# Optimization experiments

Hardware: AMD Instinct MI355X
Metric: run time of the kernel (lower is better)

Reference implementation:

```python
import jax, jax.numpy as jnp
import numpy as np

FD, NH, SP, GS = 256, 4, 2, 80.0
E = FD // NH
SP3 = SP ** 3


def _bilinear(plane, uv):
    # plane: [B,C,H,W], uv: [B,N,2] in [0,1] -> [B,C,N] (align_corners=True style)
    B, C, H, W = plane.shape
    x = jnp.clip(uv[..., 0], 0.0, 1.0) * (W - 1)
    y = jnp.clip(uv[..., 1], 0.0, 1.0) * (H - 1)
    x0 = jnp.floor(x); y0 = jnp.floor(y)
    wx = (x - x0)[:, None, :]; wy = (y - y0)[:, None, :]
    x0i = x0.astype(jnp.int32); y0i = y0.astype(jnp.int32)
    x1i = jnp.minimum(x0i + 1, W - 1); y1i = jnp.minimum(y0i + 1, H - 1)
    g = jax.vmap(lambda pl, yy, xx: pl[:, yy, xx])  # per-batch gather -> [C,N]
    f00 = g(plane, y0i, x0i); f01 = g(plane, y0i, x1i)
    f10 = g(plane, y1i, x0i); f11 = g(plane, y1i, x1i)
    return (f00 * (1 - wy) * (1 - wx) + f01 * (1 - wy) * wx
            + f10 * wy * (1 - wx) + f11 * wy * wx)


def _triplane(p, c_xz, c_xy, c_yz):
    # p: [B,N,3] in [0,1] -> [B,N,FD]; sum of three plane samples (ConvONet style)
    px, py, pz = p[..., 0], p[..., 1], p[..., 2]
    f = (_bilinear(c_xz, jnp.stack([px, pz], -1))
         + _bilinear(c_xy, jnp.stack([px, py], -1))
         + _bilinear(c_yz, jnp.stack([py, pz], -1)))
    return jnp.swapaxes(f, 1, 2)


def setup_inputs() -> dict:
    key = jax.random.key(0)
    ks = jax.random.split(key, 10)
    bs, ns, H = 4, 1024, 128
    inp = {}
    inp['query_pos'] = jax.random.uniform(ks[0], (bs, ns, 3), dtype=jnp.float32)
    for i, nm in enumerate(['c_xz', 'c_xy', 'c_yz']):
        inp[nm] = jax.random.normal(ks[1 + i], (bs, FD, H, H), dtype=jnp.float32)

    def lin(k, fi, fo):  # xavier-uniform like torch init
        lim = (6.0 / (fi + fo)) ** 0.5
        return jax.random.uniform(k, (fi, fo), minval=-lim, maxval=lim, dtype=jnp.float32)

    # to_offset: small random weight (torch inits to 0; small noise exercises the path),
    # bias = normalized sp^3 anchor grid / grid_scale, tiled over heads (as in __init__)
    inp['w_off'] = 0.01 * jax.random.normal(ks[4], (FD, SP3 * NH * 3), dtype=jnp.float32)
    g = np.stack(np.meshgrid(np.arange(SP), np.arange(SP), np.arange(SP), indexing='ij'), axis=-1).astype(np.float32)
    gsc = (2.0 * g / max(SP - 1, 1) - 1.0) / GS  # [sp,sp,sp,3]
    inp['b_off'] = jnp.asarray(np.tile(gsc[:, :, :, None, :], (1, 1, 1, NH, 1)).reshape(-1))
    inp['w_q'] = lin(ks[5], FD, E); inp['b_q'] = jnp.zeros((E,), jnp.float32)
    inp['w_k'] = lin(ks[6], FD, E); inp['b_k'] = jnp.zeros((E,), jnp.float32)
    inp['w_v'] = lin(ks[7], FD, E); inp['b_v'] = jnp.zeros((E,), jnp.float32)
    inp['w_out'] = lin(ks[8], FD, FD); inp['b_out'] = jnp.zeros((FD,), jnp.float32)
    return inp


def reference(query_pos, c_xz, c_xy, c_yz, w_off, b_off, w_q, b_q, w_k, b_k, w_v, b_v, w_out, b_out):
    bs, ns, _ = query_pos.shape
    feature = _triplane(query_pos, c_xz, c_xy, c_yz)                 # [bs,ns,FD]
    off = (feature @ w_off + b_off).reshape(bs, ns, SP3, NH, 3)
    aux = off + query_pos[:, :, None, None, :]                        # [bs,ns,SP3,NH,3]
    aux_feat = _triplane(aux.reshape(bs, -1, 3), c_xz, c_xy, c_yz)
    aux_feat = aux_feat.reshape(bs * ns, SP3, NH, FD)
    k = jnp.swapaxes(aux_feat @ w_k + b_k, 1, 2)                      # [bn,NH,SP3,E]
    v = jnp.swapaxes(aux_feat @ w_v + b_v, 1, 2)
    # note: original does q / scale with scale = E**-0.5, i.e. q * sqrt(E)
    q = (feature @ w_q + b_q).reshape(bs * ns, 1, 1, E) * (E ** 0.5)
    q = jnp.broadcast_to(q, (bs * ns, NH, 1, E))
    sim = jnp.einsum('bnid,bnjd->bnij', q, k)                         # [bn,NH,1,SP3]
    attn = jax.nn.softmax(sim, axis=-1)                               # dropout = identity (eval)
    out = jnp.einsum('bnij,bnjd->bnid', attn, v)                      # [bn,NH,1,E]
    out = jnp.swapaxes(out, 1, 2).reshape(bs, ns, NH * E)
    return out @ w_out + b_out + feature
```

## Files before the change

kernel.cpp:

```cpp
#include <hip/hip_runtime.h>
#include <math.h>

#define FD   256
#define NH   4
#define SP3  8
#define NP   32
#define EDIM 64
#define H    128
#define NS   1024
#define BS   4
#define QTF  4
#define QTE  4

#define TEX         (H*H)
#define BATCH_ELEMS (TEX*FD)
#define PAIR_B      2
#define PAIR_Q      (PAIR_B*NS)
#define PPLANE      (PAIR_B*BATCH_ELEMS)

#define WS_PLANES 0
#define WS_FEAT   (3*PPLANE)
#define WS_QK     (WS_FEAT + PAIR_Q*FD)
#define WS_AUX    (WS_QK   + PAIR_Q*FD)
#define WS_WF     (WS_AUX  + PAIR_Q*NP*3)
#define WS_PERM   (WS_WF   + PAIR_Q*NH*FD)

__device__ __forceinline__ unsigned short f2bf(float f) {
  unsigned b = __float_as_uint(f);
  return (unsigned short)((b + 0x7FFFu + ((b >> 16) & 1u)) >> 16);
}
__device__ __forceinline__ float bf2f(unsigned short u) {
  return __uint_as_float(((unsigned)u) << 16);
}

__global__ __launch_bounds__(256) void tpk2(
    const float* __restrict__ xz, const float* __restrict__ xy,
    const float* __restrict__ yz, float* __restrict__ dstAll, int b0)
{
  int bid = blockIdx.x;
  int tT = bid & 511; bid >>= 9;
  int bl = bid & 1;   bid >>= 1;
  int pl = bid;
  const float* src = pl == 0 ? xz : (pl == 1 ? xy : yz);
  float* dst = dstAll + (size_t)pl * PPLANE + (size_t)bl * BATCH_ELEMS;
  int b = b0 + bl;

  __shared__ float T[32 * 260];
  int lane = threadIdx.x & 63, w = threadIdx.x >> 6;
  int tex4 = (lane & 7) * 4;
  int csub = lane >> 3;

  const float* sbase = src + (size_t)b * FD * TEX + tT * 32;
  #pragma unroll
  for (int i = 0; i < 8; i++) {
    int c = i * 32 + w * 8 + csub;
    float4 v = *(const float4*)(sbase + (size_t)c * TEX + tex4);
    T[(tex4 + 0) * 260 + c] = v.x;
    T[(tex4 + 1) * 260 + c] = v.y;
    T[(tex4 + 2) * 260 + c] = v.z;
    T[(tex4 + 3) * 260 + c] = v.w;
  }
  __syncthreads();
  #pragma unroll
  for (int i = 0; i < 8; i++) {
    int t = w * 8 + i;
    float4 v = *(const float4*)(&T[t * 260 + lane * 4]);
    *(float4*)(dst + (size_t)(tT * 32 + t) * FD + lane * 4) = v;
  }
}

__device__ __forceinline__ unsigned mort7(unsigned v) {
  unsigned r = 0;
  #pragma unroll
  for (int i = 0; i < 7; i++) r |= ((v >> i) & 1u) << (3 * i);
  return r;
}

__global__ __launch_bounds__(1024) void sortk(
    const float* __restrict__ qpos, unsigned* __restrict__ perm)
{
  const int pair = blockIdx.x;
  const int b0 = pair * PAIR_B;
  const int t = threadIdx.x;
  __shared__ unsigned cnt[256];
  __shared__ unsigned base[256];
  if (t < 256) cnt[t] = 0;
  __syncthreads();
  unsigned myb[2];
  #pragma unroll
  for (int r = 0; r < 2; r++) {
    int i = t + r * 1024;
    size_t qg = (size_t)b0 * NS + i;
    float x = fminf(fmaxf(qpos[qg * 3 + 0], 0.f), 1.f);
    float y = fminf(fmaxf(qpos[qg * 3 + 1], 0.f), 1.f);
    float z = fminf(fmaxf(qpos[qg * 3 + 2], 0.f), 1.f);
    unsigned m = (mort7((unsigned)(x * 127.f)) << 2)
               | (mort7((unsigned)(y * 127.f)) << 1)
               |  mort7((unsigned)(z * 127.f));
    unsigned bkt = ((unsigned)(i >> 10) << 7) | (m >> 14);
    myb[r] = bkt;
    atomicAdd(&cnt[bkt], 1u);
  }
  __syncthreads();
  if (t == 0) {
    unsigned s = 0;
    for (int k = 0; k < 256; k++) { base[k] = s; s += cnt[k]; }
  }
  __syncthreads();
  #pragma unroll
  for (int r = 0; r < 2; r++) {
    int i = t + r * 1024;
    unsigned pos = atomicAdd(&base[myb[r]], 1u);
    perm[(size_t)pair * PAIR_Q + pos] = (unsigned)i;
  }
}

__device__ __forceinline__ float sample_plane(const float* __restrict__ p,
                                              float u, float v) {
  float x = fminf(fmaxf(u, 0.f), 1.f) * (float)(H - 1);
  float y = fminf(fmaxf(v, 0.f), 1.f) * (float)(H - 1);
  float xf = floorf(x), yf = floorf(y);
  int x0 = (int)xf, y0 = (int)yf;
  float wx = x - xf, wy = y - yf;
  int dx = (x0 < H - 1) ? FD : 0;
  int dy = (y0 < H - 1) ? H * FD : 0;
  int i00 = (y0 * H + x0) * FD;
  float f00 = p[i00], f01 = p[i00 + dx], f10 = p[i00 + dy], f11 = p[i00 + dy + dx];
  float a = f00 + wx * (f01 - f00);
  float b = f10 + wx * (f11 - f10);
  return a + wy * (b - a);
}

__device__ __forceinline__ void setup_samp(int* si, float* sw, float u, float v) {
  float x = fminf(fmaxf(u, 0.f), 1.f) * (float)(H - 1);
  float y = fminf(fmaxf(v, 0.f), 1.f) * (float)(H - 1);
  float xf = floorf(x), yf = floorf(y);
  int x0 = (int)xf, y0 = (int)yf;
  float wx = x - xf, wy = y - yf;
  si[0] = (y0 * H + x0) * FD;
  si[1] = (x0 < H - 1) ? FD : 0;
  si[2] = (y0 < H - 1) ? H * FD : 0;
  sw[0] = (1.f - wy) * (1.f - wx);
  sw[1] = (1.f - wy) * wx;
  sw[2] = wy * (1.f - wx);
  sw[3] = wy * wx;
}

__global__ __launch_bounds__(256) void featk(
    const float* __restrict__ qpos, const float* __restrict__ planesT,
    const float* __restrict__ w_off, const float* __restrict__ b_off,
    const float* __restrict__ w_q, const float* __restrict__ b_q,
    const float* __restrict__ w_k,
    float* __restrict__ feat, float* __restrict__ aux, float* __restrict__ qk,
    int b0)
{
  const int tid = threadIdx.x;
  const int q0l = blockIdx.x * QTF;
  const int bl = q0l >> 10;
  __shared__ float s_feat[QTF * 260];
  __shared__ float s_q[QTF * 68];

  const float* Pxz = planesT + 0 * (size_t)PPLANE + (size_t)bl * BATCH_ELEMS + tid;
  const float* Pxy = planesT + 1 * (size_t)PPLANE + (size_t)bl * BATCH_ELEMS + tid;
  const float* Pyz = planesT + 2 * (size_t)PPLANE + (size_t)bl * BATCH_ELEMS + tid;

  for (int qs = 0; qs < QTF; qs++) {
    size_t qg = (size_t)b0 * NS + q0l + qs;
    float px = qpos[qg * 3 + 0], py = qpos[qg * 3 + 1], pz = qpos[qg * 3 + 2];
    float f = sample_plane(Pxz, px, pz) + sample_plane(Pxy, px, py)
            + sample_plane(Pyz, py, pz);
    s_feat[qs * 260 + tid] = f;
    feat[(size_t)(q0l + qs) * FD + tid] = f;
  }
  __syncthreads();

  if (tid < 192) {
    int half = tid / 96, j = tid - half * 96;
    float acc[2];
    float bj = b_off[j];
    acc[0] = bj; acc[1] = bj;
    for (int c = 0; c < FD; c++) {
      float wv = w_off[c * 96 + j];
      #pragma unroll
      for (int k = 0; k < 2; k++)
        acc[k] = fmaf(s_feat[(half * 2 + k) * 260 + c], wv, acc[k]);
    }
    int d = j % 3;
    #pragma unroll
    for (int k = 0; k < 2; k++) {
      int qs = half * 2 + k;
      size_t qg = (size_t)b0 * NS + q0l + qs;
      aux[(size_t)(q0l + qs) * 96 + j] = acc[k] + qpos[qg * 3 + d];
    }
  }
  {
    int e = tid & 63, g = tid >> 6;
    float a = b_q[e];
    for (int c = 0; c < FD; c++)
      a = fmaf(s_feat[g * 260 + c], w_q[c * EDIM + e], a);
    s_q[g * 68 + e] = a * 8.0f;
  }
  __syncthreads();
  {
    float acc[QTF];
    #pragma unroll
    for (int qs = 0; qs < QTF; qs++) acc[qs] = 0.f;
    const float4* wk4 = reinterpret_cast<const float4*>(w_k + (size_t)tid * EDIM);
    for (int e4 = 0; e4 < EDIM / 4; e4++) {
      float4 wv = wk4[e4];
      int e = e4 * 4;
      #pragma unroll
      for (int qs = 0; qs < QTF; qs++) {
        acc[qs] = fmaf(s_q[qs * 68 + e + 0], wv.x, acc[qs]);
        acc[qs] = fmaf(s_q[qs * 68 + e + 1], wv.y, acc[qs]);
        acc[qs] = fmaf(s_q[qs * 68 + e + 2], wv.z, acc[qs]);
        acc[qs] = fmaf(s_q[qs * 68 + e + 3], wv.w, acc[qs]);
      }
    }
    #pragma unroll
    for (int qs = 0; qs < QTF; qs++)
      qk[(size_t)(q0l + qs) * FD + tid] = acc[qs];
  }
}

__global__ __launch_bounds__(256, 6) void attnk(
    const float* __restrict__ planesT, const float* __restrict__ aux,
    const float* __restrict__ qk, const unsigned* __restrict__ perm,
    float* __restrict__ wf)
{
  const int tid = threadIdx.x, lane = tid & 63, w = tid >> 6;
  const int bid = blockIdx.x;
  const int j = ((bid & 7) << 8) | (bid >> 3);
  const int c4 = lane * 4;

  __shared__ int   s_si[96][3];
  __shared__ float s_sw[96][4];

  const int qw = (int)perm[j];
  const int blw = qw >> 10;

  if (tid < 96) {
    int p = tid / 3, pl = tid - p * 3;
    float ax = aux[(size_t)qw * 96 + p * 3 + 0];
    float ay = aux[(size_t)qw * 96 + p * 3 + 1];
    float az = aux[(size_t)qw * 96 + p * 3 + 2];
    float u = (pl == 2) ? ay : ax;
    float v = (pl == 1) ? ay : az;
    setup_samp(s_si[tid], s_sw[tid], u, v);
  }

  const int h = w;
  float4 qk4 = *(const float4*)(qk + (size_t)qw * FD + c4);
  const float* P0 = planesT + 0 * (size_t)PPLANE + (size_t)blw * BATCH_ELEMS + c4;
  const float* P1 = planesT + 1 * (size_t)PPLANE + (size_t)blw * BATCH_ELEMS + c4;
  const float* P2 = planesT + 2 * (size_t)PPLANE + (size_t)blw * BATCH_ELEMS + c4;
  __syncthreads();

  ushort4 af16[SP3];
  float t[SP3];
  float4 acc;

  float4 bA00, bA01, bA10, bA11;
  float4 bB00, bB01, bB10, bB11;

  auto issue = [&](int k, float4& b00, float4& b01, float4& b10, float4& b11) {
    const int pl = k % 3;
    const int p  = (k / 3) * NH + h;
    const float* P = pl == 0 ? P0 : (pl == 1 ? P1 : P2);
    int i00 = s_si[p * 3 + pl][0];
    int dxo = s_si[p * 3 + pl][1];
    int dyo = s_si[p * 3 + pl][2];
    b00 = *(const float4*)(P + i00);
    b01 = *(const float4*)(P + i00 + dxo);
    b10 = *(const float4*)(P + i00 + dyo);
    b11 = *(const float4*)(P + i00 + dyo + dxo);
  };
  auto consume = [&](int k, float4& b00, float4& b01, float4& b10, float4& b11) {
    const int pl = k % 3, jj = k / 3;
    const int p  = jj * NH + h;
    float w0 = s_sw[p * 3 + pl][0], w1 = s_sw[p * 3 + pl][1];
    float w2 = s_sw[p * 3 + pl][2], w3 = s_sw[p * 3 + pl][3];
    if (pl == 0) { acc.x = 0.f; acc.y = 0.f; acc.z = 0.f; acc.w = 0.f; }
    acc.x = fmaf(w0, b00.x, fmaf(w1, b01.x, fmaf(w2, b10.x, fmaf(w3, b11.x, acc.x))));
    acc.y = fmaf(w0, b00.y, fmaf(w1, b01.y, fmaf(w2, b10.y, fmaf(w3, b11.y, acc.y))));
    acc.z = fmaf(w0, b00.z, fmaf(w1, b01.z, fmaf(w2, b10.z, fmaf(w3, b11.z, acc.z))));
    acc.w = fmaf(w0, b00.w, fmaf(w1, b01.w, fmaf(w2, b10.w, fmaf(w3, b11.w, acc.w))));
    if (pl == 2) {
      ushort4 hh;
      hh.x = f2bf(acc.x); hh.y = f2bf(acc.y); hh.z = f2bf(acc.z); hh.w = f2bf(acc.w);
      af16[jj] = hh;
      t[jj] = fmaf(qk4.x, acc.x, fmaf(qk4.y, acc.y, fmaf(qk4.z, acc.z, qk4.w * acc.w)));
    }
  };

  issue(0, bA00, bA01, bA10, bA11);
  #pragma unroll
  for (int k = 0; k < 24; k += 2) {
    if (k + 1 < 24) issue(k + 1, bB00, bB01, bB10, bB11);
    consume(k, bA00, bA01, bA10, bA11);
    if (k + 2 < 24) issue(k + 2, bA00, bA01, bA10, bA11);
    if (k + 1 < 24) consume(k + 1, bB00, bB01, bB10, bB11);
  }

  #pragma unroll
  for (int o = 32; o >= 1; o >>= 1) {
    #pragma unroll
    for (int jj = 0; jj < SP3; jj++) t[jj] += __shfl_xor(t[jj], o, 64);
  }

  float m = -1e30f;
  #pragma unroll
  for (int jj = 0; jj < SP3; jj++) m = fmaxf(m, t[jj]);
  float sum = 0.f;
  #pragma unroll
  for (int jj = 0; jj < SP3; jj++) { t[jj] = __expf(t[jj] - m); sum += t[jj]; }
  float inv = 1.0f / sum;
  float4 r; r.x = 0.f; r.y = 0.f; r.z = 0.f; r.w = 0.f;
  #pragma unroll
  for (int jj = 0; jj < SP3; jj++) {
    float av = t[jj] * inv;
    ushort4 hv = af16[jj];
    r.x = fmaf(av, bf2f(hv.x), r.x);
    r.y = fmaf(av, bf2f(hv.y), r.y);
    r.z = fmaf(av, bf2f(hv.z), r.z);
    r.w = fmaf(av, bf2f(hv.w), r.w);
  }
  *(float4*)(wf + ((size_t)qw * NH + h) * FD + c4) = r;
}

__global__ __launch_bounds__(256) void epik(
    const float* __restrict__ wf, const float* __restrict__ feat,
    const float* __restrict__ w_v, const float* __restrict__ b_v,
    const float* __restrict__ w_out, const float* __restrict__ b_out,
    float* __restrict__ out, int b0)
{
  const int tid = threadIdx.x;
  const int q0l = blockIdx.x * QTE;
  __shared__ float s_wv[FD * EDIM];
  __shared__ float s_o[QTE * 257];

  {
    const float4* src4 = (const float4*)w_v;
    float4* dst4 = (float4*)s_wv;
    #pragma unroll
    for (int i = 0; i < (FD * EDIM / 4) / 256; i++)
      dst4[tid + 256 * i] = src4[tid + 256 * i];
  }
  __syncthreads();

  {
    int h = tid >> 6, e = tid & 63;
    float acc[QTE];
    float bv = b_v[e];
    #pragma unroll
    for (int qs = 0; qs < QTE; qs++) acc[qs] = bv;
    const float* wrow = wf + ((size_t)q0l * NH + h) * FD;
    for (int c = 0; c < FD; c++) {
      float wv = s_wv[c * EDIM + e];
      #pragma unroll
      for (int qs = 0; qs < QTE; qs++)
        acc[qs] = fmaf(wrow[(size_t)qs * NH * FD + c], wv, acc[qs]);
    }
    #pragma unroll
    for (int qs = 0; qs < QTE; qs++) s_o[qs * 257 + h * EDIM + e] = acc[qs];
  }
  __syncthreads();

  {
    float r[QTE];
    float bo = b_out[tid];
    #pragma unroll
    for (int qs = 0; qs < QTE; qs++) r[qs] = bo;
    for (int c = 0; c < FD; c++) {
      float wv = w_out[(size_t)c * FD + tid];
      #pragma unroll
      for (int qs = 0; qs < QTE; qs++)
        r[qs] = fmaf(s_o[qs * 257 + c], wv, r[qs]);
    }
    #pragma unroll
    for (int qs = 0; qs < QTE; qs++)
      out[((size_t)b0 * NS + q0l + qs) * FD + tid]
          = r[qs] + feat[(size_t)(q0l + qs) * FD + tid];
  }
}

extern "C" void kernel_launch(void* const* d_in, const int* in_sizes, int n_in,
                              void* d_out, int out_size, void* d_ws, size_t ws_size,
                              hipStream_t stream) {
  const float* qp    = (const float*)d_in[0];
  const float* cxz   = (const float*)d_in[1];
  const float* cxy   = (const float*)d_in[2];
  const float* cyz   = (const float*)d_in[3];
  const float* w_off = (const float*)d_in[4];
  const float* b_off = (const float*)d_in[5];
  const float* w_q   = (const float*)d_in[6];
  const float* b_q   = (const float*)d_in[7];
  const float* w_k   = (const float*)d_in[8];
  const float* b_k   = (const float*)d_in[9];   (void)b_k;
  const float* w_v   = (const float*)d_in[10];
  const float* b_v   = (const float*)d_in[11];
  const float* w_out = (const float*)d_in[12];
  const float* b_out = (const float*)d_in[13];
  float* out = (float*)d_out;
  (void)in_sizes; (void)n_in; (void)out_size; (void)ws_size;

  float* ws      = (float*)d_ws;
  float* planesT = ws + WS_PLANES;
  float* feat    = ws + WS_FEAT;
  float* qk      = ws + WS_QK;
  float* aux     = ws + WS_AUX;
  float* wf      = ws + WS_WF;
  unsigned* perm = (unsigned*)(ws + WS_PERM);

  hipLaunchKernelGGL(sortk, dim3(BS / PAIR_B), dim3(1024), 0, stream, qp, perm);

  for (int pair = 0; pair < BS / PAIR_B; ++pair) {
    int b0 = pair * PAIR_B;
    hipLaunchKernelGGL(tpk2, dim3(3 * PAIR_B * 512), dim3(256), 0, stream,
                       cxz, cxy, cyz, planesT, b0);
    hipLaunchKernelGGL(featk, dim3(PAIR_Q / QTF), dim3(256), 0, stream,
                       qp, planesT, w_off, b_off, w_q, b_q, w_k,
                       feat, aux, qk, b0);
    hipLaunchKernelGGL(attnk, dim3(PAIR_Q), dim3(256), 0, stream,
                       planesT, aux, qk, perm + (size_t)pair * PAIR_Q, wf);
    hipLaunchKernelGGL(epik, dim3(PAIR_Q / QTE), dim3(256), 0, stream,
                       wf, feat, w_v, b_v, w_out, b_out, out, b0);
  }
}
```

Before: 514.6 us.

## Fuse feature, attention and epilogue kernels into one per-query kernel

Merges featk, attnk and epik into one kernel that handles one query per block. The triplane feature, offsets, q, qk, attention-weighted features and both output projections now stay in shared memory, which removes the global round trips through the feat/aux/qk/wf buffers and two launches per pair. In exchange, the weight matrices (w_off, w_q, w_k, w_v, w_out) are read once per query instead of being amortized over 4 queries per block. The w_v shared-memory staging is also dropped, so the block's matvec work and global weight traffic go up.

```diff
diff --git a/kernel.cpp b/kernel.cpp
--- a/kernel.cpp
+++ b/kernel.cpp
@@ -9,8 +9,6 @@
 #define H    128
 #define NS   1024
 #define BS   4
-#define QTF  4
-#define QTE  4
 
 #define TEX         (H*H)
 #define BATCH_ELEMS (TEX*FD)
@@ -146,115 +144,90 @@
   sw[3] = wy * wx;
 }
 
-__global__ __launch_bounds__(256) void featk(
+__global__ __launch_bounds__(256, 8) void fusedk(
     const float* __restrict__ qpos, const float* __restrict__ planesT,
     const float* __restrict__ w_off, const float* __restrict__ b_off,
     const float* __restrict__ w_q, const float* __restrict__ b_q,
     const float* __restrict__ w_k,
-    float* __restrict__ feat, float* __restrict__ aux, float* __restrict__ qk,
-    int b0)
-{
-  const int tid = threadIdx.x;
-  const int q0l = blockIdx.x * QTF;
-  const int bl = q0l >> 10;
-  __shared__ float s_feat[QTF * 260];
-  __shared__ float s_q[QTF * 68];
-
-  const float* Pxz = planesT + 0 * (size_t)PPLANE + (size_t)bl * BATCH_ELEMS + tid;
-  const float* Pxy = planesT + 1 * (size_t)PPLANE + (size_t)bl * BATCH_ELEMS + tid;
-  const float* Pyz = planesT + 2 * (size_t)PPLANE + (size_t)bl * BATCH_ELEMS + tid;
-
-  for (int qs = 0; qs < QTF; qs++) {
-    size_t qg = (size_t)b0 * NS + q0l + qs;
-    float px = qpos[qg * 3 + 0], py = qpos[qg * 3 + 1], pz = qpos[qg * 3 + 2];
-    float f = sample_plane(Pxz, px, pz) + sample_plane(Pxy, px, py)
-            + sample_plane(Pyz, py, pz);
-    s_feat[qs * 260 + tid] = f;
-    feat[(size_t)(q0l + qs) * FD + tid] = f;
-  }
-  __syncthreads();
-
-  if (tid < 192) {
-    int half = tid / 96, j = tid - half * 96;
-    float acc[2];
-    float bj = b_off[j];
-    acc[0] = bj; acc[1] = bj;
-    for (int c = 0; c < FD; c++) {
-      float wv = w_off[c * 96 + j];
-      #pragma unroll
-      for (int k = 0; k < 2; k++)
-        acc[k] = fmaf(s_feat[(half * 2 + k) * 260 + c], wv, acc[k]);
-    }
-    int d = j % 3;
-    #pragma unroll
-    for (int k = 0; k < 2; k++) {
-      int qs = half * 2 + k;
-      size_t qg = (size_t)b0 * NS + q0l + qs;
-      aux[(size_t)(q0l + qs) * 96 + j] = acc[k] + qpos[qg * 3 + d];
-    }
-  }
-  {
-    int e = tid & 63, g = tid >> 6;
-    float a = b_q[e];
-    for (int c = 0; c < FD; c++)
-      a = fmaf(s_feat[g * 260 + c], w_q[c * EDIM + e], a);
-    s_q[g * 68 + e] = a * 8.0f;
-  }
-  __syncthreads();
-  {
-    float acc[QTF];
-    #pragma unroll
-    for (int qs = 0; qs < QTF; qs++) acc[qs] = 0.f;
-    const float4* wk4 = reinterpret_cast<const float4*>(w_k + (size_t)tid * EDIM);
-    for (int e4 = 0; e4 < EDIM / 4; e4++) {
-      float4 wv = wk4[e4];
-      int e = e4 * 4;
-      #pragma unroll
-      for (int qs = 0; qs < QTF; qs++) {
-        acc[qs] = fmaf(s_q[qs * 68 + e + 0], wv.x, acc[qs]);
-        acc[qs] = fmaf(s_q[qs * 68 + e + 1], wv.y, acc[qs]);
-        acc[qs] = fmaf(s_q[qs * 68 + e + 2], wv.z, acc[qs]);
-        acc[qs] = fmaf(s_q[qs * 68 + e + 3], wv.w, acc[qs]);
-      }
-    }
-    #pragma unroll
-    for (int qs = 0; qs < QTF; qs++)
-      qk[(size_t)(q0l + qs) * FD + tid] = acc[qs];
-  }
-}
-
-__global__ __launch_bounds__(256, 6) void attnk(
-    const float* __restrict__ planesT, const float* __restrict__ aux,
-    const float* __restrict__ qk, const unsigned* __restrict__ perm,
-    float* __restrict__ wf)
+    const float* __restrict__ w_v, const float* __restrict__ b_v,
+    const float* __restrict__ w_out, const float* __restrict__ b_out,
+    const unsigned* __restrict__ perm, float* __restrict__ out, int b0)
 {
   const int tid = threadIdx.x, lane = tid & 63, w = tid >> 6;
   const int bid = blockIdx.x;
   const int j = ((bid & 7) << 8) | (bid >> 3);
   const int c4 = lane * 4;
 
+  __shared__ float s_feat[FD];
+  __shared__ float s_aux[96];
+  __shared__ float s_q[EDIM];
+  __shared__ float s_qk[FD];
   __shared__ int   s_si[96][3];
   __shared__ float s_sw[96][4];
+  __shared__ float s_wf[NH * FD];
+  __shared__ float s_o[FD];
 
   const int qw = (int)perm[j];
   const int blw = qw >> 10;
-
+  const size_t qg = (size_t)b0 * NS + qw;
+  const float px = qpos[qg * 3 + 0];
+  const float py = qpos[qg * 3 + 1];
+  const float pz = qpos[qg * 3 + 2];
+
+  const float* Pxz = planesT + 0 * (size_t)PPLANE + (size_t)blw * BATCH_ELEMS;
+  const float* Pxy = planesT + 1 * (size_t)PPLANE + (size_t)blw * BATCH_ELEMS;
+  const float* Pyz = planesT + 2 * (size_t)PPLANE + (size_t)blw * BATCH_ELEMS;
+
+  {
+    float f = sample_plane(Pxz + tid, px, pz) + sample_plane(Pxy + tid, px, py)
+            + sample_plane(Pyz + tid, py, pz);
+    s_feat[tid] = f;
+  }
+  __syncthreads();
+
+  if (tid < 160) {
+    const bool isOff = tid < 96;
+    const int  col   = isOff ? tid : (tid - 96);
+    const float* Wp  = isOff ? (w_off + col) : (w_q + col);
+    const int  strd  = isOff ? 96 : EDIM;
+    float acc = isOff ? b_off[col] : b_q[col];
+    for (int c = 0; c < FD; c++) {
+      acc = fmaf(s_feat[c], *Wp, acc);
+      Wp += strd;
+    }
+    if (isOff) {
+      int d = col % 3;
+      float qp = (d == 0) ? px : ((d == 1) ? py : pz);
+      s_aux[col] = acc + qp;
+    } else {
+      s_q[col] = acc * 8.0f;
+    }
+  }
+  __syncthreads();
+
+  {
+    float acc = 0.f;
+    const float* wk = w_k + (size_t)tid * EDIM;
+    for (int e = 0; e < EDIM; e++)
+      acc = fmaf(s_q[e], wk[e], acc);
+    s_qk[tid] = acc;
+  }
   if (tid < 96) {
     int p = tid / 3, pl = tid - p * 3;
-    float ax = aux[(size_t)qw * 96 + p * 3 + 0];
-    float ay = aux[(size_t)qw * 96 + p * 3 + 1];
-    float az = aux[(size_t)qw * 96 + p * 3 + 2];
+    float ax = s_aux[p * 3 + 0];
+    float ay = s_aux[p * 3 + 1];
+    float az = s_aux[p * 3 + 2];
     float u = (pl == 2) ? ay : ax;
     float v = (pl == 1) ? ay : az;
     setup_samp(s_si[tid], s_sw[tid], u, v);
   }
+  __syncthreads();
 
   const int h = w;
-  float4 qk4 = *(const float4*)(qk + (size_t)qw * FD + c4);
-  const float* P0 = planesT + 0 * (size_t)PPLANE + (size_t)blw * BATCH_ELEMS + c4;
-  const float* P1 = planesT + 1 * (size_t)PPLANE + (size_t)blw * BATCH_ELEMS + c4;
-  const float* P2 = planesT + 2 * (size_t)PPLANE + (size_t)blw * BATCH_ELEMS + c4;
-  __syncthreads();
+  float4 qk4 = *(const float4*)(s_qk + c4);
+  const float* P0 = Pxz + c4;
+  const float* P1 = Pxy + c4;
+  const float* P2 = Pyz + c4;
 
   ushort4 af16[SP3];
   float t[SP3];
@@ -325,62 +298,24 @@
     r.z = fmaf(av, bf2f(hv.z), r.z);
     r.w = fmaf(av, bf2f(hv.w), r.w);
   }
-  *(float4*)(wf + ((size_t)qw * NH + h) * FD + c4) = r;
-}
-
-__global__ __launch_bounds__(256) void epik(
-    const float* __restrict__ wf, const float* __restrict__ feat,
-    const float* __restrict__ w_v, const float* __restrict__ b_v,
-    const float* __restrict__ w_out, const float* __restrict__ b_out,
-    float* __restrict__ out, int b0)
-{
-  const int tid = threadIdx.x;
-  const int q0l = blockIdx.x * QTE;
-  __shared__ float s_wv[FD * EDIM];
-  __shared__ float s_o[QTE * 257];
+  *(float4*)(s_wf + h * FD + c4) = r;
+  __syncthreads();
 
   {
-    const float4* src4 = (const float4*)w_v;
-    float4* dst4 = (float4*)s_wv;
-    #pragma unroll
-    for (int i = 0; i < (FD * EDIM / 4) / 256; i++)
-      dst4[tid + 256 * i] = src4[tid + 256 * i];
+    const int hh = tid >> 6, e = tid & 63;
+    float a5 = b_v[e];
+    const float* wrow = s_wf + hh * FD;
+    for (int c = 0; c < FD; c++)
+      a5 = fmaf(wrow[c], w_v[(size_t)c * EDIM + e], a5);
+    s_o[tid] = a5;
   }
   __syncthreads();
 
   {
-    int h = tid >> 6, e = tid & 63;
-    float acc[QTE];
-    float bv = b_v[e];
-    #pragma unroll
-    for (int qs = 0; qs < QTE; qs++) acc[qs] = bv;
-    const float* wrow = wf + ((size_t)q0l * NH + h) * FD;
-    for (int c = 0; c < FD; c++) {
-      float wv = s_wv[c * EDIM + e];
-      #pragma unroll
-      for (int qs = 0; qs < QTE; qs++)
-        acc[qs] = fmaf(wrow[(size_t)qs * NH * FD + c], wv, acc[qs]);
-    }
-    #pragma unroll
-    for (int qs = 0; qs < QTE; qs++) s_o[qs * 257 + h * EDIM + e] = acc[qs];
-  }
-  __syncthreads();
-
-  {
-    float r[QTE];
-    float bo = b_out[tid];
-    #pragma unroll
-    for (int qs = 0; qs < QTE; qs++) r[qs] = bo;
-    for (int c = 0; c < FD; c++) {
-      float wv = w_out[(size_t)c * FD + tid];
-      #pragma unroll
-      for (int qs = 0; qs < QTE; qs++)
-        r[qs] = fmaf(s_o[qs * 257 + c], wv, r[qs]);
-    }
-    #pragma unroll
-    for (int qs = 0; qs < QTE; qs++)
-      out[((size_t)b0 * NS + q0l + qs) * FD + tid]
-          = r[qs] + feat[(size_t)(q0l + qs) * FD + tid];
+    float r5 = b_out[tid];
+    for (int c = 0; c < FD; c++)
+      r5 = fmaf(s_o[c], w_out[(size_t)c * FD + tid], r5);
+    out[qg * FD + tid] = r5 + s_feat[tid];
   }
 }
 
@@ -406,10 +341,6 @@
 
   float* ws      = (float*)d_ws;
   float* planesT = ws + WS_PLANES;
-  float* feat    = ws + WS_FEAT;
-  float* qk      = ws + WS_QK;
-  float* aux     = ws + WS_AUX;
-  float* wf      = ws + WS_WF;
   unsigned* perm = (unsigned*)(ws + WS_PERM);
 
   hipLaunchKernelGGL(sortk, dim3(BS / PAIR_B), dim3(1024), 0, stream, qp, perm);
@@ -418,12 +349,9 @@
     int b0 = pair * PAIR_B;
     hipLaunchKernelGGL(tpk2, dim3(3 * PAIR_B * 512), dim3(256), 0, stream,
                        cxz, cxy, cyz, planesT, b0);
-    hipLaunchKernelGGL(featk, dim3(PAIR_Q / QTF), dim3(256), 0, stream,
+    hipLaunchKernelGGL(fusedk, dim3(PAIR_Q), dim3(256), 0, stream,
                        qp, planesT, w_off, b_off, w_q, b_q, w_k,
-                       feat, aux, qk, b0);
-    hipLaunchKernelGGL(attnk, dim3(PAIR_Q), dim3(256), 0, stream,
-                       planesT, aux, qk, perm + (size_t)pair * PAIR_Q, wf);
-    hipLaunchKernelGGL(epik, dim3(PAIR_Q / QTE), dim3(256), 0, stream,
-                       wf, feat, w_v, b_v, w_out, b_out, out, b0);
-  }
-}
+                       w_v, b_v, w_out, b_out,
+                       perm + (size_t)pair * PAIR_Q, out, b0);
+  }
+}
```

Measured after the change: 485.4 us. -5.7%, faster.
